# Performance work log

Measured on AMD Instinct MI355X. Metric: run time of the kernel, lower is better.

The kernel has to match this reference:

```python
import math
import jax, jax.numpy as jnp
import numpy as np

B, T, D, H = 1, 4096, 1024, 16
HD = D // H  # 64

def setup_inputs() -> dict:
    key = jax.random.key(0)
    k1, k2, k3 = jax.random.split(key, 3)
    x = jax.random.normal(k1, (B, T, D), dtype=jnp.float32)
    # torch nn.Linear weight layout: [out_features, in_features]
    w_attn = jax.random.normal(k2, (3 * D, D), dtype=jnp.float32) * (1.0 / math.sqrt(D))
    w_proj = jax.random.normal(k3, (D, D), dtype=jnp.float32) * (1.0 / math.sqrt(D))
    return {"x": x, "w_attn": w_attn, "w_proj": w_proj}

def reference(x, w_attn, w_proj):
    b, t, d = x.shape
    qkv = jnp.einsum('btd,ed->bte', x, w_attn)  # [B,T,3D]
    q, k, v = jnp.split(qkv, 3, axis=-1)
    # [B,H,T,HD]
    q = q.reshape(b, t, H, HD).transpose(0, 2, 1, 3)
    k = k.reshape(b, t, H, HD).transpose(0, 2, 1, 3)
    v = v.reshape(b, t, H, HD).transpose(0, 2, 1, 3)
    scale = 1.0 / math.sqrt(HD)
    att = jnp.einsum('bhqd,bhkd->bhqk', q, k) * scale  # [B,H,T,T]
    causal = jnp.tril(jnp.ones((t, t), dtype=bool))
    att = jnp.where(causal[None, None], att, -jnp.inf)
    att = jax.nn.softmax(att, axis=-1)
    y = jnp.einsum('bhqk,bhkd->bhqd', att, v)  # [B,H,T,HD]
    y = y.transpose(0, 2, 1, 3).reshape(b, t, d)
    return jnp.einsum('btd,ed->bte', y, w_proj)
```

## Files before the change

### kernel.cpp

```cpp
#include <hip/hip_runtime.h>
#include <hip/hip_bf16.h>

typedef __bf16 bf16x8 __attribute__((ext_vector_type(8)));
typedef float  f32x4  __attribute__((ext_vector_type(4)));

__device__ __forceinline__ void async_load16(const void* g, void* l) {
    __builtin_amdgcn_global_load_lds(
        (const __attribute__((address_space(1))) unsigned int*)g,
        (__attribute__((address_space(3))) unsigned int*)l,
        16, 0, 0);
}

__device__ __forceinline__ bool sniff_is_bf16(const void* src) {
    const unsigned int* p = (const unsigned int*)src;
    unsigned v = p[threadIdx.x & 63];
    unsigned e = (v >> 7) & 0xFF;
    unsigned long long m = __ballot(e >= 100 && e <= 140);
    return __popcll(m) >= 48;
}

__global__ __launch_bounds__(256) void to_bf16(const void* __restrict__ src,
                                               __bf16* __restrict__ dst, int n) {
    bool b16 = sniff_is_bf16(src);
    int i = (blockIdx.x * 256 + threadIdx.x) * 4;
    if (i >= n) return;
    if (b16) {
        *(uint2*)(dst + i) = *(const uint2*)((const __bf16*)src + i);
    } else {
        float4 v = *(const float4*)((const float*)src + i);
        dst[i]     = (__bf16)v.x;
        dst[i + 1] = (__bf16)v.y;
        dst[i + 2] = (__bf16)v.z;
        dst[i + 3] = (__bf16)v.w;
    }
}

__global__ __launch_bounds__(256) void gemm_bt(
    const __bf16* __restrict__ A,
    const __bf16* __restrict__ B,
    void* __restrict__ Cv,
    int M, int N, int K,
    const void* sniff)
{
    bool out_b16 = true;
    if (sniff) out_b16 = sniff_is_bf16(sniff);

    __shared__ __bf16 As[128 * 32];
    __shared__ __bf16 Bs[128 * 32];

    const int tid  = threadIdx.x;
    const int lane = tid & 63;
    const int w    = tid >> 6;
    const int wm   = w >> 1, wn = w & 1;
    const int m0   = blockIdx.y * 128;
    const int n0   = blockIdx.x * 128;
    const int c    = lane & 15;
    const int g    = lane >> 4;

    f32x4 acc[4][4] = {};

    const int e0 = tid * 8;
    const int e1 = e0 + 2048;
    const int r0 = e0 >> 5, c0 = e0 & 31;
    const int r1 = e1 >> 5, c1 = e1 & 31;

    for (int k0 = 0; k0 < K; k0 += 32) {
        async_load16(A + (size_t)(m0 + r0) * K + k0 + c0, As + e0);
        async_load16(A + (size_t)(m0 + r1) * K + k0 + c1, As + e1);
        async_load16(B + (size_t)(n0 + r0) * K + k0 + c0, Bs + e0);
        async_load16(B + (size_t)(n0 + r1) * K + k0 + c1, Bs + e1);
        __syncthreads();

        bf16x8 af[4], bfr[4];
        #pragma unroll
        for (int i = 0; i < 4; i++)
            af[i] = *(const bf16x8*)&As[(wm * 64 + i * 16 + c) * 32 + g * 8];
        #pragma unroll
        for (int j = 0; j < 4; j++)
            bfr[j] = *(const bf16x8*)&Bs[(wn * 64 + j * 16 + c) * 32 + g * 8];
        #pragma unroll
        for (int i = 0; i < 4; i++)
            #pragma unroll
            for (int j = 0; j < 4; j++)
                acc[i][j] = __builtin_amdgcn_mfma_f32_16x16x32_bf16(af[i], bfr[j], acc[i][j], 0, 0, 0);
        __syncthreads();
    }

    #pragma unroll
    for (int i = 0; i < 4; i++) {
        const int row0 = m0 + wm * 64 + i * 16 + g * 4;
        #pragma unroll
        for (int j = 0; j < 4; j++) {
            const int col = n0 + wn * 64 + j * 16 + c;
            #pragma unroll
            for (int r = 0; r < 4; r++) {
                const size_t idx = (size_t)(row0 + r) * N + col;
                if (out_b16) ((__bf16*)Cv)[idx] = (__bf16)acc[i][j][r];
                else         ((float*)Cv)[idx]  = acc[i][j][r];
            }
        }
    }
}

__global__ __launch_bounds__(256) void vtrans(const __bf16* __restrict__ qkv,
                                              __bf16* __restrict__ vT) {
    __shared__ __bf16 Lt[64 * 72];
    const int tid = threadIdx.x;
    const int h   = blockIdx.y;
    const int t0  = blockIdx.x * 64;
    #pragma unroll
    for (int rr = 0; rr < 2; rr++) {
        int e = rr * 2048 + tid * 8;
        int tr = e >> 6, tc = e & 63;
        bf16x8 v = *(const bf16x8*)&qkv[(size_t)(t0 + tr) * 3072 + 2048 + h * 64 + tc];
        #pragma unroll
        for (int i = 0; i < 8; i++) Lt[(tc + i) * 72 + tr] = v[i];
    }
    __syncthreads();
    #pragma unroll
    for (int rr = 0; rr < 2; rr++) {
        int e = rr * 2048 + tid * 8;
        int dr = e >> 6, dc = e & 63;
        *(bf16x8*)&vT[(size_t)h * 262144 + (size_t)dr * 4096 + t0 + dc]
            = *(const bf16x8*)&Lt[dr * 72 + dc];
    }
}

__global__ __launch_bounds__(256, 3) void attn_fwd(
    const __bf16* __restrict__ qkv,
    const __bf16* __restrict__ vT,
    __bf16* __restrict__ y)
{
    constexpr int LDQ = 3072;
    constexpr float SCL = 0.18033688011112042f;
    constexpr float MEXP = 16.0f;
    __shared__ __bf16 Ks[2][64 * 64];
    __shared__ __bf16 Vs[2][64 * 64];
    __shared__ __bf16 Ps[4][16 * 72];

    const int id   = blockIdx.x;
    const int h    = (id & 7) * 2 + (id >> 9);
    const int qt   = 63 - ((id >> 3) & 63);
    const int tid  = threadIdx.x;
    const int lane = tid & 63;
    const int w    = tid >> 6;
    const int c    = lane & 15;
    const int g    = lane >> 4;
    const int qoff = h * 64;
    const int qs   = qt * 64;
    const int nkt  = qt + 1;

    const int p0 = tid, p1 = tid + 256;
    const int sr0 = p0 >> 3, sg0 = ((p0 & 7) ^ (sr0 & 7)) * 8;
    const int sr1 = p1 >> 3, sg1 = ((p1 & 7) ^ (sr1 & 7)) * 8;
    const __bf16* vbase = vT + (size_t)h * 262144;

    int cur = 0;
    async_load16(qkv + (size_t)sr0 * LDQ + 1024 + qoff + sg0, &Ks[0][p0 * 8]);
    async_load16(qkv + (size_t)sr1 * LDQ + 1024 + qoff + sg1, &Ks[0][p1 * 8]);
    async_load16(vbase + (size_t)sr0 * 4096 + sg0, &Vs[0][p0 * 8]);
    async_load16(vbase + (size_t)sr1 * 4096 + sg1, &Vs[0][p1 * 8]);

    bf16x8 qf[2];
    {
        const __bf16* qrow = qkv + (size_t)(qs + w * 16 + c) * LDQ + qoff;
        bf16x8 q0 = *(const bf16x8*)(qrow + g * 8);
        bf16x8 q1 = *(const bf16x8*)(qrow + 32 + g * 8);
        #pragma unroll
        for (int i = 0; i < 8; i++) {
            qf[0][i] = (__bf16)((float)q0[i] * SCL);
            qf[1][i] = (__bf16)((float)q1[i] * SCL);
        }
    }

    float l_lane = 0.f;
    f32x4 o[4] = {};

    for (int t = 0; t < nkt; t++) {
        __syncthreads();

        if (t + 1 < nkt) {
            const int nks = (t + 1) * 64;
            const int nb = cur ^ 1;
            async_load16(qkv + (size_t)(nks + sr0) * LDQ + 1024 + qoff + sg0, &Ks[nb][p0 * 8]);
            async_load16(qkv + (size_t)(nks + sr1) * LDQ + 1024 + qoff + sg1, &Ks[nb][p1 * 8]);
            async_load16(vbase + (size_t)sr0 * 4096 + nks + sg0, &Vs[nb][p0 * 8]);
            async_load16(vbase + (size_t)sr1 * 4096 + nks + sg1, &Vs[nb][p1 * 8]);
        }

        const __bf16* ks_ = Ks[cur];
        const __bf16* vs_ = Vs[cur];

        f32x4 sa[4] = {};
        #pragma unroll
        for (int s = 0; s < 2; s++) {
            #pragma unroll
            for (int j = 0; j < 4; j++) {
                bf16x8 kf = *(const bf16x8*)&ks_[(j * 16 + c) * 64 + ((s * 4 + g) ^ (c & 7)) * 8];
                sa[j] = __builtin_amdgcn_mfma_f32_16x16x32_bf16(kf, qf[s], sa[j], 0, 0, 0);
            }
        }

        if (t == nkt - 1) {
            #pragma unroll
            for (int j = 0; j < 4; j++)
                #pragma unroll
                for (int r = 0; r < 4; r++)
                    if (j * 16 + g * 4 + r > w * 16 + c) sa[j][r] = -1e30f;
        }

        __bf16* pw = &Ps[w][0];
        #pragma unroll
        for (int j = 0; j < 4; j++) {
            __bf16 pb[4] __attribute__((aligned(8)));
            #pragma unroll
            for (int r = 0; r < 4; r++) {
                float p = __builtin_amdgcn_exp2f(sa[j][r] - MEXP);
                l_lane += p;
                pb[r] = (__bf16)p;
            }
            *(uint2*)&pw[c * 72 + j * 16 + g * 4] = *(const uint2*)pb;
        }

        #pragma unroll
        for (int s = 0; s < 2; s++) {
            bf16x8 pf = *(const bf16x8*)&pw[c * 72 + s * 32 + g * 8];
            #pragma unroll
            for (int j = 0; j < 4; j++) {
                bf16x8 vf = *(const bf16x8*)&vs_[(j * 16 + c) * 64 + ((s * 4 + g) ^ (c & 7)) * 8];
                o[j] = __builtin_amdgcn_mfma_f32_16x16x32_bf16(vf, pf, o[j], 0, 0, 0);
            }
        }
        cur ^= 1;
    }

    float l_run = l_lane;
    l_run += __shfl_xor(l_run, 16);
    l_run += __shfl_xor(l_run, 32);

    const float rl = 1.0f / l_run;
    #pragma unroll
    for (int j = 0; j < 4; j++) {
        __bf16 ob[4] __attribute__((aligned(8)));
        #pragma unroll
        for (int r = 0; r < 4; r++) ob[r] = (__bf16)(o[j][r] * rl);
        *(uint2*)&y[(size_t)(qs + w * 16 + c) * 1024 + qoff + j * 16 + g * 4]
            = *(const uint2*)ob;
    }
}

extern "C" void kernel_launch(void* const* d_in, const int* in_sizes, int n_in,
                              void* d_out, int out_size, void* d_ws, size_t ws_size,
                              hipStream_t stream) {
    constexpr int T = 4096, D = 1024;

    __bf16* cx   = (__bf16*)d_ws;
    __bf16* cwa  = cx  + (size_t)T * D;
    __bf16* cwp  = cwa + (size_t)3 * D * D;
    __bf16* qkv  = cwp + (size_t)D * D;
    __bf16* y    = qkv + (size_t)T * 3 * D;
    __bf16* vT   = cx;

    to_bf16<<<T * D / 1024, 256, 0, stream>>>(d_in[0], cx, T * D);
    to_bf16<<<3 * D * D / 1024, 256, 0, stream>>>(d_in[1], cwa, 3 * D * D);
    to_bf16<<<D * D / 1024, 256, 0, stream>>>(d_in[2], cwp, D * D);

    gemm_bt<<<dim3(3 * D / 128, T / 128), 256, 0, stream>>>(cx, cwa, qkv, T, 3 * D, D, nullptr);
    vtrans<<<dim3(T / 64, 16), 256, 0, stream>>>(qkv, vT);
    attn_fwd<<<1024, 256, 0, stream>>>(qkv, vT, y);
    gemm_bt<<<dim3(D / 128, T / 128), 256, 0, stream>>>(y, cwp, d_out, T, D, D, d_in[2]);
}
```

Measured before the change: 232.4 us.

## Process 128 query rows per attention block to reuse K/V tiles

Each attention workgroup now handles a 128-row query tile, with each wave owning 32 rows instead of 16, so every K/V tile loaded into LDS feeds twice as many MFMAs. This halves the grid to 512 blocks and cuts total K/V global and LDS traffic. In exchange it doubles accumulator and P-buffer state per wave, which raises register pressure, and the causal mask now applies to the last two key tiles. With fewer, larger blocks, load balance and occupancy across the 256 CUs may suffer.

```diff
diff --git a/kernel.cpp b/kernel.cpp
--- a/kernel.cpp
+++ b/kernel.cpp
@@ -136,19 +136,19 @@
     constexpr float MEXP = 16.0f;
     __shared__ __bf16 Ks[2][64 * 64];
     __shared__ __bf16 Vs[2][64 * 64];
-    __shared__ __bf16 Ps[4][16 * 72];
+    __shared__ __bf16 Ps[4][32 * 72];
 
     const int id   = blockIdx.x;
-    const int h    = (id & 7) * 2 + (id >> 9);
-    const int qt   = 63 - ((id >> 3) & 63);
+    const int h    = (id & 7) * 2 + (id >> 8);
+    const int qt   = 31 - ((id >> 3) & 31);
     const int tid  = threadIdx.x;
     const int lane = tid & 63;
     const int w    = tid >> 6;
     const int c    = lane & 15;
     const int g    = lane >> 4;
     const int qoff = h * 64;
-    const int qs   = qt * 64;
-    const int nkt  = qt + 1;
+    const int qs   = qt * 128;
+    const int nkt  = 2 * qt + 2;
 
     const int p0 = tid, p1 = tid + 256;
     const int sr0 = p0 >> 3, sg0 = ((p0 & 7) ^ (sr0 & 7)) * 8;
@@ -161,20 +161,21 @@
     async_load16(vbase + (size_t)sr0 * 4096 + sg0, &Vs[0][p0 * 8]);
     async_load16(vbase + (size_t)sr1 * 4096 + sg1, &Vs[0][p1 * 8]);
 
-    bf16x8 qf[2];
-    {
-        const __bf16* qrow = qkv + (size_t)(qs + w * 16 + c) * LDQ + qoff;
+    bf16x8 qf[2][2];
+    #pragma unroll
+    for (int qq = 0; qq < 2; qq++) {
+        const __bf16* qrow = qkv + (size_t)(qs + w * 32 + qq * 16 + c) * LDQ + qoff;
         bf16x8 q0 = *(const bf16x8*)(qrow + g * 8);
         bf16x8 q1 = *(const bf16x8*)(qrow + 32 + g * 8);
         #pragma unroll
         for (int i = 0; i < 8; i++) {
-            qf[0][i] = (__bf16)((float)q0[i] * SCL);
-            qf[1][i] = (__bf16)((float)q1[i] * SCL);
-        }
-    }
-
-    float l_lane = 0.f;
-    f32x4 o[4] = {};
+            qf[qq][0][i] = (__bf16)((float)q0[i] * SCL);
+            qf[qq][1][i] = (__bf16)((float)q1[i] * SCL);
+        }
+    }
+
+    float l_lane[2] = {0.f, 0.f};
+    f32x4 o[2][4] = {};
 
     for (int t = 0; t < nkt; t++) {
         __syncthreads();
@@ -191,61 +192,72 @@
         const __bf16* ks_ = Ks[cur];
         const __bf16* vs_ = Vs[cur];
 
-        f32x4 sa[4] = {};
+        f32x4 sa[2][4] = {};
         #pragma unroll
         for (int s = 0; s < 2; s++) {
             #pragma unroll
             for (int j = 0; j < 4; j++) {
                 bf16x8 kf = *(const bf16x8*)&ks_[(j * 16 + c) * 64 + ((s * 4 + g) ^ (c & 7)) * 8];
-                sa[j] = __builtin_amdgcn_mfma_f32_16x16x32_bf16(kf, qf[s], sa[j], 0, 0, 0);
-            }
-        }
-
-        if (t == nkt - 1) {
-            #pragma unroll
-            for (int j = 0; j < 4; j++)
+                sa[0][j] = __builtin_amdgcn_mfma_f32_16x16x32_bf16(kf, qf[0][s], sa[0][j], 0, 0, 0);
+                sa[1][j] = __builtin_amdgcn_mfma_f32_16x16x32_bf16(kf, qf[1][s], sa[1][j], 0, 0, 0);
+            }
+        }
+
+        if (t + 2 >= nkt) {
+            const int kb = t * 64 - qs;
+            #pragma unroll
+            for (int qq = 0; qq < 2; qq++)
                 #pragma unroll
-                for (int r = 0; r < 4; r++)
-                    if (j * 16 + g * 4 + r > w * 16 + c) sa[j][r] = -1e30f;
+                for (int j = 0; j < 4; j++)
+                    #pragma unroll
+                    for (int r = 0; r < 4; r++)
+                        if (kb + j * 16 + g * 4 + r > w * 32 + qq * 16 + c) sa[qq][j][r] = -1e30f;
         }
 
         __bf16* pw = &Ps[w][0];
         #pragma unroll
-        for (int j = 0; j < 4; j++) {
-            __bf16 pb[4] __attribute__((aligned(8)));
-            #pragma unroll
-            for (int r = 0; r < 4; r++) {
-                float p = __builtin_amdgcn_exp2f(sa[j][r] - MEXP);
-                l_lane += p;
-                pb[r] = (__bf16)p;
-            }
-            *(uint2*)&pw[c * 72 + j * 16 + g * 4] = *(const uint2*)pb;
+        for (int qq = 0; qq < 2; qq++) {
+            #pragma unroll
+            for (int j = 0; j < 4; j++) {
+                __bf16 pb[4] __attribute__((aligned(8)));
+                #pragma unroll
+                for (int r = 0; r < 4; r++) {
+                    float p = __builtin_amdgcn_exp2f(sa[qq][j][r] - MEXP);
+                    l_lane[qq] += p;
+                    pb[r] = (__bf16)p;
+                }
+                *(uint2*)&pw[(qq * 16 + c) * 72 + j * 16 + g * 4] = *(const uint2*)pb;
+            }
         }
 
         #pragma unroll
         for (int s = 0; s < 2; s++) {
-            bf16x8 pf = *(const bf16x8*)&pw[c * 72 + s * 32 + g * 8];
+            bf16x8 pf0 = *(const bf16x8*)&pw[c * 72 + s * 32 + g * 8];
+            bf16x8 pf1 = *(const bf16x8*)&pw[(16 + c) * 72 + s * 32 + g * 8];
             #pragma unroll
             for (int j = 0; j < 4; j++) {
                 bf16x8 vf = *(const bf16x8*)&vs_[(j * 16 + c) * 64 + ((s * 4 + g) ^ (c & 7)) * 8];
-                o[j] = __builtin_amdgcn_mfma_f32_16x16x32_bf16(vf, pf, o[j], 0, 0, 0);
+                o[0][j] = __builtin_amdgcn_mfma_f32_16x16x32_bf16(vf, pf0, o[0][j], 0, 0, 0);
+                o[1][j] = __builtin_amdgcn_mfma_f32_16x16x32_bf16(vf, pf1, o[1][j], 0, 0, 0);
             }
         }
         cur ^= 1;
     }
 
-    float l_run = l_lane;
-    l_run += __shfl_xor(l_run, 16);
-    l_run += __shfl_xor(l_run, 32);
-
-    const float rl = 1.0f / l_run;
-    #pragma unroll
-    for (int j = 0; j < 4; j++) {
-        __bf16 ob[4] __attribute__((aligned(8)));
-        #pragma unroll
-        for (int r = 0; r < 4; r++) ob[r] = (__bf16)(o[j][r] * rl);
-        *(uint2*)&y[(size_t)(qs + w * 16 + c) * 1024 + qoff + j * 16 + g * 4]
-            = *(const uint2*)ob;
+    #pragma unroll
+    for (int qq = 0; qq < 2; qq++) {
+        float l_run = l_lane[qq];
+        l_run += __shfl_xor(l_run, 16);
+        l_run += __shfl_xor(l_run, 32);
+        const float rl = 1.0f / l_run;
+        #pragma unroll
+        for (int j = 0; j < 4; j++) {
+            __bf16 ob[4] __attribute__((aligned(8)));
+            #pragma unroll
+            for (int r = 0; r < 4; r++) ob[r] = (__bf16)(o[qq][j][r] * rl);
+            *(uint2*)&y[(size_t)(qs + w * 32 + qq * 16 + c) * 1024 + qoff + j * 16 + g * 4]
+                = *(const uint2*)ob;
+        }
     }
 }
 
@@ -267,6 +279,6 @@
 
     gemm_bt<<<dim3(3 * D / 128, T / 128), 256, 0, stream>>>(cx, cwa, qkv, T, 3 * D, D, nullptr);
     vtrans<<<dim3(T / 64, 16), 256, 0, stream>>>(qkv, vT);
-    attn_fwd<<<1024, 256, 0, stream>>>(qkv, vT, y);
+    attn_fwd<<<512, 256, 0, stream>>>(qkv, vT, y);
     gemm_bt<<<dim3(D / 128, T / 128), 256, 0, stream>>>(y, cwp, d_out, T, D, D, d_in[2]);
 }
```

Result: slower. 254.3 us (+9.5%).

## Split QK^T across waves by key rows and share P tile through LDS

Applied to the files above, without the earlier changes.

Each wave now computes scores for all 64 query rows against its own 16-key slice, so it reads one K fragment per step instead of four while keeping all four Q fragments in registers. The probabilities are written to a shared, XOR-swizzled 64x64 P tile, and after a block barrier each wave reads its query rows for the PV product. Row sums are reduced across waves through LDS at the end. This cuts K reads from LDS but adds a block-wide barrier every iteration and more registers for Q, which can lower occupancy.

```diff
diff --git a/kernel.cpp b/kernel.cpp
--- a/kernel.cpp
+++ b/kernel.cpp
@@ -136,7 +136,7 @@
     constexpr float MEXP = 16.0f;
     __shared__ __bf16 Ks[2][64 * 64];
     __shared__ __bf16 Vs[2][64 * 64];
-    __shared__ __bf16 Ps[4][16 * 72];
+    __shared__ __bf16 Ps[64 * 64];
 
     const int id   = blockIdx.x;
     const int h    = (id & 7) * 2 + (id >> 9);
@@ -149,6 +149,7 @@
     const int qoff = h * 64;
     const int qs   = qt * 64;
     const int nkt  = qt + 1;
+    const int xq   = (c & 7) << 1;
 
     const int p0 = tid, p1 = tid + 256;
     const int sr0 = p0 >> 3, sg0 = ((p0 & 7) ^ (sr0 & 7)) * 8;
@@ -161,19 +162,20 @@
     async_load16(vbase + (size_t)sr0 * 4096 + sg0, &Vs[0][p0 * 8]);
     async_load16(vbase + (size_t)sr1 * 4096 + sg1, &Vs[0][p1 * 8]);
 
-    bf16x8 qf[2];
-    {
-        const __bf16* qrow = qkv + (size_t)(qs + w * 16 + c) * LDQ + qoff;
+    bf16x8 qf[4][2];
+    #pragma unroll
+    for (int n = 0; n < 4; n++) {
+        const __bf16* qrow = qkv + (size_t)(qs + n * 16 + c) * LDQ + qoff;
         bf16x8 q0 = *(const bf16x8*)(qrow + g * 8);
         bf16x8 q1 = *(const bf16x8*)(qrow + 32 + g * 8);
         #pragma unroll
         for (int i = 0; i < 8; i++) {
-            qf[0][i] = (__bf16)((float)q0[i] * SCL);
-            qf[1][i] = (__bf16)((float)q1[i] * SCL);
-        }
-    }
-
-    float l_lane = 0.f;
+            qf[n][0][i] = (__bf16)((float)q0[i] * SCL);
+            qf[n][1][i] = (__bf16)((float)q1[i] * SCL);
+        }
+    }
+
+    float l_lane[4] = {};
     f32x4 o[4] = {};
 
     for (int t = 0; t < nkt; t++) {
@@ -194,37 +196,39 @@
         f32x4 sa[4] = {};
         #pragma unroll
         for (int s = 0; s < 2; s++) {
-            #pragma unroll
-            for (int j = 0; j < 4; j++) {
-                bf16x8 kf = *(const bf16x8*)&ks_[(j * 16 + c) * 64 + ((s * 4 + g) ^ (c & 7)) * 8];
-                sa[j] = __builtin_amdgcn_mfma_f32_16x16x32_bf16(kf, qf[s], sa[j], 0, 0, 0);
-            }
+            bf16x8 kf = *(const bf16x8*)&ks_[(w * 16 + c) * 64 + ((s * 4 + g) ^ (c & 7)) * 8];
+            #pragma unroll
+            for (int n = 0; n < 4; n++)
+                sa[n] = __builtin_amdgcn_mfma_f32_16x16x32_bf16(kf, qf[n][s], sa[n], 0, 0, 0);
         }
 
         if (t == nkt - 1) {
             #pragma unroll
-            for (int j = 0; j < 4; j++)
+            for (int n = 0; n < 4; n++)
                 #pragma unroll
                 for (int r = 0; r < 4; r++)
-                    if (j * 16 + g * 4 + r > w * 16 + c) sa[j][r] = -1e30f;
-        }
-
-        __bf16* pw = &Ps[w][0];
-        #pragma unroll
-        for (int j = 0; j < 4; j++) {
+                    if (w * 16 + g * 4 + r > n * 16 + c) sa[n][r] = -1e30f;
+        }
+
+        #pragma unroll
+        for (int n = 0; n < 4; n++) {
             __bf16 pb[4] __attribute__((aligned(8)));
             #pragma unroll
             for (int r = 0; r < 4; r++) {
-                float p = __builtin_amdgcn_exp2f(sa[j][r] - MEXP);
-                l_lane += p;
+                float p = __builtin_amdgcn_exp2f(sa[n][r] - MEXP);
+                l_lane[n] += p;
                 pb[r] = (__bf16)p;
             }
-            *(uint2*)&pw[c * 72 + j * 16 + g * 4] = *(const uint2*)pb;
-        }
+            *(uint2*)&Ps[(n * 16 + c) * 64 + ((w * 4 + g) ^ xq) * 4] = *(const uint2*)pb;
+        }
+
+        asm volatile("s_waitcnt lgkmcnt(0)" ::: "memory");
+        __builtin_amdgcn_s_barrier();
+        asm volatile("" ::: "memory");
 
         #pragma unroll
         for (int s = 0; s < 2; s++) {
-            bf16x8 pf = *(const bf16x8*)&pw[c * 72 + s * 32 + g * 8];
+            bf16x8 pf = *(const bf16x8*)&Ps[(w * 16 + c) * 64 + ((s * 8 + g * 2) ^ xq) * 4];
             #pragma unroll
             for (int j = 0; j < 4; j++) {
                 bf16x8 vf = *(const bf16x8*)&vs_[(j * 16 + c) * 64 + ((s * 4 + g) ^ (c & 7)) * 8];
@@ -234,9 +238,20 @@
         cur ^= 1;
     }
 
-    float l_run = l_lane;
-    l_run += __shfl_xor(l_run, 16);
-    l_run += __shfl_xor(l_run, 32);
+    #pragma unroll
+    for (int n = 0; n < 4; n++) {
+        l_lane[n] += __shfl_xor(l_lane[n], 16);
+        l_lane[n] += __shfl_xor(l_lane[n], 32);
+    }
+    __syncthreads();
+    float* ls = (float*)Ps;
+    if (g == 0) {
+        #pragma unroll
+        for (int n = 0; n < 4; n++) ls[(w * 4 + n) * 16 + c] = l_lane[n];
+    }
+    __syncthreads();
+    float l_run = ls[(0 * 4 + w) * 16 + c] + ls[(1 * 4 + w) * 16 + c]
+                + ls[(2 * 4 + w) * 16 + c] + ls[(3 * 4 + w) * 16 + c];
 
     const float rl = 1.0f / l_run;
     #pragma unroll
```

After: 239.9 us. +3.3%, slower.
